# Kernel tuning notes

Hardware: AMD Instinct MI355X
Metric: run time of the kernel (lower is better)

## Reference

```python
import jax, jax.numpy as jnp
import numpy as np

H = 128
N_USER, N_PC, N_URL = 100000, 20000, 50000
E_UP, E_UU = 250000, 500000
NUM_LAYERS = 2


def _sage(x_src, x_dst, src_idx, dst_idx, n_dst, Wl, bl, Wr):
    # PyG SAGEConv (aggr='mean', root_weight=True, lin_r bias=False):
    # out = lin_l(mean_j x_src[j]) + lin_r(x_dst)
    msg = x_src[src_idx]                                   # [E, H] gather
    agg = jax.ops.segment_sum(msg, dst_idx, num_segments=n_dst)
    cnt = jax.ops.segment_sum(jnp.ones((src_idx.shape[0], 1), x_src.dtype),
                              dst_idx, num_segments=n_dst)
    mean = agg / jnp.maximum(cnt, 1.0)
    return mean @ Wl + bl + x_dst @ Wr


def setup_inputs() -> dict:
    key = jax.random.key(0)
    ks = jax.random.split(key, 24)
    s = 0.05
    inp = {
        'x_user': jax.random.normal(ks[0], (N_USER, 6), jnp.float32),
        'x_pc': jax.random.normal(ks[1], (N_PC, 4), jnp.float32),
        'x_url': jax.random.normal(ks[2], (N_URL, 3), jnp.float32),
        'edge_up_src': jax.random.randint(ks[3], (E_UP,), 0, N_USER, jnp.int32),
        'edge_up_dst': jax.random.randint(ks[4], (E_UP,), 0, N_PC, jnp.int32),
        'edge_uu_src': jax.random.randint(ks[5], (E_UU,), 0, N_USER, jnp.int32),
        'edge_uu_dst': jax.random.randint(ks[6], (E_UU,), 0, N_URL, jnp.int32),
        # input projections
        'Wu': jax.random.normal(ks[7], (6, H), jnp.float32) * s,
        'bu': jnp.zeros((H,), jnp.float32),
        'Wp': jax.random.normal(ks[8], (4, H), jnp.float32) * s,
        'bp': jnp.zeros((H,), jnp.float32),
        'Wr_feat': jax.random.normal(ks[9], (3, H), jnp.float32) * s,
        'br_feat': jnp.zeros((H,), jnp.float32),
        # SAGEConv params, stacked over layers [L, H, H]
        'Wl_pc': jax.random.normal(ks[10], (NUM_LAYERS, H, H), jnp.float32) * s,
        'bl_pc': jnp.zeros((NUM_LAYERS, H), jnp.float32),
        'Wr_pc': jax.random.normal(ks[11], (NUM_LAYERS, H, H), jnp.float32) * s,
        'Wl_url': jax.random.normal(ks[12], (NUM_LAYERS, H, H), jnp.float32) * s,
        'bl_url': jnp.zeros((NUM_LAYERS, H), jnp.float32),
        'Wr_url': jax.random.normal(ks[13], (NUM_LAYERS, H, H), jnp.float32) * s,
        # context aggregation + classifier
        'Wctx': jax.random.normal(ks[14], (3 * H, H), jnp.float32) * s,
        'bctx': jnp.zeros((H,), jnp.float32),
        'Wc1': jax.random.normal(ks[15], (H, H // 2), jnp.float32) * s,
        'bc1': jnp.zeros((H // 2,), jnp.float32),
        'Wc2': jax.random.normal(ks[16], (H // 2, 2), jnp.float32) * s,
        'bc2': jnp.zeros((2,), jnp.float32),
    }
    return inp


def reference(x_user, x_pc, x_url,
              edge_up_src, edge_up_dst, edge_uu_src, edge_uu_dst,
              Wu, bu, Wp, bp, Wr_feat, br_feat,
              Wl_pc, bl_pc, Wr_pc, Wl_url, bl_url, Wr_url,
              Wctx, bctx, Wc1, bc1, Wc2, bc2):
    user = x_user @ Wu + bu          # [N_USER, H] (never updated by convs)
    pc = x_pc @ Wp + bp              # [N_PC, H]
    url = x_url @ Wr_feat + br_feat  # [N_URL, H]

    for i in range(NUM_LAYERS):
        pc_new = _sage(user, pc, edge_up_src, edge_up_dst, pc.shape[0],
                       Wl_pc[i], bl_pc[i], Wr_pc[i])
        url_new = _sage(user, url, edge_uu_src, edge_uu_dst, url.shape[0],
                        Wl_url[i], bl_url[i], Wr_url[i])
        if i == 0:
            pc = jax.nn.relu(pc_new)
            url = jax.nn.relu(url_new)
        else:
            pc = jax.nn.relu(pc_new + pc)
            url = jax.nn.relu(url_new + url)

    # aggregate_resource_context: scatter-add of resource embeddings into users
    pc_ctx = jax.ops.segment_sum(pc[edge_up_dst], edge_up_src, num_segments=user.shape[0])
    url_ctx = jax.ops.segment_sum(url[edge_uu_dst], edge_uu_src, num_segments=user.shape[0])
    combined = jnp.concatenate([user, pc_ctx, url_ctx], axis=1)   # [N_USER, 3H]
    enriched = combined @ Wctx + bctx

    # classifier (dropout inactive at inference)
    h = jax.nn.relu(enriched @ Wc1 + bc1)
    return h @ Wc2 + bc2
```

## Files before the change

### kernel.cpp

```cpp
#include <hip/hip_runtime.h>

typedef unsigned short u16;
typedef short short8_t __attribute__((ext_vector_type(8)));
typedef float floatx4 __attribute__((ext_vector_type(4)));

static constexpr int N_USER_C = 100000;
static constexpr int N_PC_C   = 20000;
static constexpr int N_URL_C  = 50000;
static constexpr int E_UP_C   = 250000;
static constexpr int E_UU_C   = 500000;

static constexpr int S_UPD = 48;
static constexpr int S_UUD = 40;
static constexpr int S_SRC = 24;

__device__ __forceinline__ float bf2f(u16 h) {
    return __uint_as_float(((unsigned)h) << 16);
}
__device__ __forceinline__ u16 f2bf(float f) {
    unsigned u = __float_as_uint(f);
    u += 0x7fffu + ((u >> 16) & 1u);
    return (u16)(u >> 16);
}

struct PFArgs {
    const float* wsrc[12];
    u16* wdst;
    const float *Xu, *Wu, *bu, *Xp, *Wp, *bp, *Xr, *Wr, *br;
    u16 *ou, *op, *orr;
    const int *up_src, *up_dst, *uu_src, *uu_dst;
    int *cnt_up_dst, *cnt_uu_dst, *cnt_up_src, *cnt_uu_src;
    int *val_up_dst, *val_uu_dst;
    u16 *val_up_src, *val_uu_src;
};
__global__ __launch_bounds__(256) void prepfill_kernel(PFArgs a)
{
    int b = blockIdx.x, tid = threadIdx.x;
    if (b < 1960) {
        const int range = b & 7;
        const int ebase = (b >> 3) * 2048 + tid;
#pragma unroll
        for (int i = 0; i < 8; ++i) {
            int e = ebase + i * 256;
            if (e < E_UP_C) {
                int s = __builtin_nontemporal_load(a.up_src + e);
                int d = __builtin_nontemporal_load(a.up_dst + e);
                if (d / 2500 == range) {
                    int p = atomicAdd(&a.cnt_up_dst[d], 1);
                    if (p < S_UPD) a.val_up_dst[d * S_UPD + p] = s;
                }
                if (s / 12500 == range) {
                    int p = atomicAdd(&a.cnt_up_src[s], 1);
                    if (p < S_SRC) a.val_up_src[s * S_SRC + p] = (u16)d;
                }
            }
            if (e < E_UU_C) {
                int s = __builtin_nontemporal_load(a.uu_src + e);
                int d = __builtin_nontemporal_load(a.uu_dst + e);
                if (d / 6250 == range) {
                    int p = atomicAdd(&a.cnt_uu_dst[d], 1);
                    if (p < S_UUD) a.val_uu_dst[d * S_UUD + p] = s;
                }
                if (s / 12500 == range) {
                    int p = atomicAdd(&a.cnt_uu_src[s], 1);
                    if (p < S_SRC) a.val_uu_src[s * S_SRC + p] = (u16)d;
                }
            }
        }
    } else if (b < 1960 + 768) {
        int idx = (b - 1960) * 256 + tid;
        int m = idx >> 14, e = idx & 16383;
        int n = e >> 7, k = e & 127;
        int Nm = (m == 11) ? 64 : 128;
        u16 v = 0;
        if (n < Nm) v = f2bf(a.wsrc[m][k * Nm + n]);
        a.wdst[(size_t)m * 16384 + n * 128 + k] = v;
    } else {
        int idx = (b - 1960 - 768) * 256 + tid;
        const float* X; const float* W; const float* bi; u16* o; int K;
        if (idx < 1600000)       { X = a.Xu; W = a.Wu; bi = a.bu; o = a.ou; K = 6; }
        else if (idx < 1920000)  { idx -= 1600000; X = a.Xp; W = a.Wp; bi = a.bp; o = a.op; K = 4; }
        else                     { idx -= 1920000; X = a.Xr; W = a.Wr; bi = a.br; o = a.orr; K = 3; }
        int r = idx >> 4, c0 = (idx & 15) * 8;
        float acc[8];
        {
            const float4 b0 = *(const float4*)(bi + c0);
            const float4 b1 = *(const float4*)(bi + c0 + 4);
            acc[0] = b0.x; acc[1] = b0.y; acc[2] = b0.z; acc[3] = b0.w;
            acc[4] = b1.x; acc[5] = b1.y; acc[6] = b1.z; acc[7] = b1.w;
        }
        for (int k = 0; k < K; ++k) {
            float xk = X[(size_t)r * K + k];
            const float4 w0 = *(const float4*)(W + k * 128 + c0);
            const float4 w1 = *(const float4*)(W + k * 128 + c0 + 4);
            acc[0] += xk * w0.x; acc[1] += xk * w0.y; acc[2] += xk * w0.z; acc[3] += xk * w0.w;
            acc[4] += xk * w1.x; acc[5] += xk * w1.y; acc[6] += xk * w1.z; acc[7] += xk * w1.w;
        }
        uint4 pk;
        pk.x = (unsigned)f2bf(acc[0]) | ((unsigned)f2bf(acc[1]) << 16);
        pk.y = (unsigned)f2bf(acc[2]) | ((unsigned)f2bf(acc[3]) << 16);
        pk.z = (unsigned)f2bf(acc[4]) | ((unsigned)f2bf(acc[5]) << 16);
        pk.w = (unsigned)f2bf(acc[6]) | ((unsigned)f2bf(acc[7]) << 16);
        *(uint4*)(o + (size_t)r * 128 + c0) = pk;
    }
}

__device__ __forceinline__ void gm_row(
    const u16* __restrict__ feat, const int* __restrict__ cnt,
    const int* __restrict__ vals, int stride, u16* __restrict__ outp, int row, int lane)
{
    int deg = cnt[row];
    deg = __builtin_amdgcn_readfirstlane(deg);
    int n = deg < stride ? deg : stride;
    const int* vp = vals + row * stride;
    float a0 = 0.f, a1 = 0.f, b0 = 0.f, b1 = 0.f;
    float c0 = 0.f, c1 = 0.f, d0 = 0.f, d1 = 0.f;
    int j = 0;
    for (; j + 4 <= n; j += 4) {
        int i0 = __builtin_nontemporal_load(vp + j);
        int i1 = __builtin_nontemporal_load(vp + j + 1);
        int i2 = __builtin_nontemporal_load(vp + j + 2);
        int i3 = __builtin_nontemporal_load(vp + j + 3);
        unsigned u0 = *(const unsigned*)(feat + (size_t)i0 * 128 + lane * 2);
        unsigned u1 = *(const unsigned*)(feat + (size_t)i1 * 128 + lane * 2);
        unsigned u2 = *(const unsigned*)(feat + (size_t)i2 * 128 + lane * 2);
        unsigned u3 = *(const unsigned*)(feat + (size_t)i3 * 128 + lane * 2);
        a0 += bf2f((u16)(u0 & 0xffff)); a1 += bf2f((u16)(u0 >> 16));
        b0 += bf2f((u16)(u1 & 0xffff)); b1 += bf2f((u16)(u1 >> 16));
        c0 += bf2f((u16)(u2 & 0xffff)); c1 += bf2f((u16)(u2 >> 16));
        d0 += bf2f((u16)(u3 & 0xffff)); d1 += bf2f((u16)(u3 >> 16));
    }
    for (; j < n; ++j) {
        int i0 = __builtin_nontemporal_load(vp + j);
        unsigned u0 = *(const unsigned*)(feat + (size_t)i0 * 128 + lane * 2);
        a0 += bf2f((u16)(u0 & 0xffff)); a1 += bf2f((u16)(u0 >> 16));
    }
    float ax = (a0 + b0) + (c0 + d0), ay = (a1 + b1) + (c1 + d1);
    float inv = 1.0f / fmaxf((float)deg, 1.0f);
    unsigned o = (unsigned)f2bf(ax * inv) | ((unsigned)f2bf(ay * inv) << 16);
    *(unsigned*)(outp + (size_t)row * 128 + lane * 2) = o;
}

__global__ __launch_bounds__(256) void mean_ctx_kernel(
    const u16* __restrict__ feat,
    const int* __restrict__ cnt_pc, const int* __restrict__ val_pc, u16* __restrict__ out_pc,
    const int* __restrict__ cnt_url, const int* __restrict__ val_url, u16* __restrict__ out_url,
    const u16* __restrict__ Wctx_t, const float* __restrict__ bctx, u16* __restrict__ enr)
{
    __shared__ u16 Ws[2][128 * 40];
    const int b = blockIdx.x, tid = threadIdx.x;
    const int wave = tid >> 6, lane = tid & 63;

    if (b >= 782) {
        int bg = b - 782;
        if (bg < 5000) gm_row(feat, cnt_pc, val_pc, S_UPD, out_pc, bg * 4 + wave, lane);
        else           gm_row(feat, cnt_url, val_url, S_UUD, out_url, (bg - 5000) * 4 + wave, lane);
        return;
    }

    const int m = lane & 15, kq = lane >> 4;
    const int rbase = b * 128 + wave * 32;
    const int sn = tid >> 1, spart = tid & 1;
    const int M = N_USER_C;

    floatx4 acc[2][8];
#pragma unroll
    for (int mt = 0; mt < 2; ++mt)
#pragma unroll
        for (int nt = 0; nt < 8; ++nt) acc[mt][nt] = (floatx4)0.0f;

    auto stageW = [&](int kc, int buf) {
        *(short8_t*)&Ws[buf][sn * 40 + spart * 16] =
            *(const short8_t*)(Wctx_t + (size_t)sn * 128 + kc + spart * 16);
        *(short8_t*)&Ws[buf][sn * 40 + spart * 16 + 8] =
            *(const short8_t*)(Wctx_t + (size_t)sn * 128 + kc + spart * 16 + 8);
    };
    auto loadA = [&](int kc, int mt) -> short8_t {
        int row = rbase + mt * 16 + m; row = row < M ? row : M - 1;
        return *(const short8_t*)(feat + (size_t)row * 128 + kc + kq * 8);
    };

    stageW(0, 0);
    short8_t an0 = loadA(0, 0), an1 = loadA(0, 1);
    __syncthreads();
    for (int c = 0; c < 4; ++c) {
        int c1 = c + 1;
        if (c1 < 4) stageW(c1 * 32, c1 & 1);
        short8_t a0 = an0, a1 = an1;
        if (c1 < 4) { an0 = loadA(c1 * 32, 0); an1 = loadA(c1 * 32, 1); }
#pragma unroll
        for (int nt = 0; nt < 8; ++nt) {
            short8_t bb = *(const short8_t*)&Ws[c & 1][(nt * 16 + m) * 40 + kq * 8];
            acc[0][nt] = __builtin_amdgcn_mfma_f32_16x16x32_bf16(a0, bb, acc[0][nt], 0, 0, 0);
            acc[1][nt] = __builtin_amdgcn_mfma_f32_16x16x32_bf16(a1, bb, acc[1][nt], 0, 0, 0);
        }
        __syncthreads();
    }
#pragma unroll
    for (int nt = 0; nt < 8; ++nt) {
        int col = nt * 16 + m;
        float bv = bctx[col];
#pragma unroll
        for (int mt = 0; mt < 2; ++mt)
#pragma unroll
            for (int r = 0; r < 4; ++r) {
                int row = rbase + mt * 16 + kq * 4 + r;
                if (row < M) enr[(size_t)row * 128 + col] = f2bf(acc[mt][nt][r] + bv);
            }
    }
}

struct FSeg {
    const u16 *mean, *x0;
    const u16 *Wl0, *Wr0, *Wl1, *Wr1, *Wc;
    const float *b0, *b1;
    u16* out; int M; int bstart;
};
struct FArgs { FSeg s[2]; };

__global__ __launch_bounds__(256) void chain_kernel(FArgs fa)
{
    constexpr int XP = 136;
    __shared__ u16 Ws[2][128 * 40];
    __shared__ u16 Xs[128 * XP];

    int si = ((int)blockIdx.x >= fa.s[1].bstart) ? 1 : 0;
    FSeg sg = fa.s[si];
    const int bb = blockIdx.x - sg.bstart;

    const int tid = threadIdx.x;
    const int wave = tid >> 6, lane = tid & 63;
    const int m = lane & 15, kq = lane >> 4;
    const int rloc = wave * 32;
    const int rbase = bb * 128 + rloc;
    const int sn = tid >> 1, spart = tid & 1;

    floatx4 acc[2][8];

    auto zeroAcc = [&]() {
#pragma unroll
        for (int mt = 0; mt < 2; ++mt)
#pragma unroll
            for (int nt = 0; nt < 8; ++nt) acc[mt][nt] = (floatx4)0.0f;
    };
    auto stageW = [&](const u16* Wt, int kc, int buf) {
        *(short8_t*)&Ws[buf][sn * 40 + spart * 16] =
            *(const short8_t*)(Wt + (size_t)sn * 128 + kc + spart * 16);
        *(short8_t*)&Ws[buf][sn * 40 + spart * 16 + 8] =
            *(const short8_t*)(Wt + (size_t)sn * 128 + kc + spart * 16 + 8);
    };
    auto loadAg = [&](const u16* A, int kc, int mt) -> short8_t {
        int row = rbase + mt * 16 + m; row = row < sg.M ? row : sg.M - 1;
        return *(const short8_t*)(A + (size_t)row * 128 + kc + kq * 8);
    };
    auto loadAs = [&](int kc, int mt) -> short8_t {
        return *(const short8_t*)&Xs[(rloc + mt * 16 + m) * XP + kc + kq * 8];
    };
    auto mfmaChunk = [&](short8_t a0, short8_t a1, int buf) {
#pragma unroll
        for (int nt = 0; nt < 8; ++nt) {
            short8_t b = *(const short8_t*)&Ws[buf][(nt * 16 + m) * 40 + kq * 8];
            acc[0][nt] = __builtin_amdgcn_mfma_f32_16x16x32_bf16(a0, b, acc[0][nt], 0, 0, 0);
            acc[1][nt] = __builtin_amdgcn_mfma_f32_16x16x32_bf16(a1, b, acc[1][nt], 0, 0, 0);
        }
    };
    auto passDual = [&](const u16* W1, const u16* A1g, const u16* W2, const u16* A2g, bool a2lds) {
        zeroAcc();
        stageW(W1, 0, 0);
        short8_t an0 = loadAg(A1g, 0, 0), an1 = loadAg(A1g, 0, 1);
        __syncthreads();
        for (int c = 0; c < 8; ++c) {
            int c1 = c + 1;
            if (c1 < 8) {
                int kc1 = (c1 & 3) * 32;
                stageW(c1 < 4 ? W1 : W2, kc1, c1 & 1);
            }
            short8_t a0 = an0, a1 = an1;
            if (c1 < 8) {
                int kc1 = (c1 & 3) * 32;
                if (c1 < 4)     { an0 = loadAg(A1g, kc1, 0); an1 = loadAg(A1g, kc1, 1); }
                else if (a2lds) { an0 = loadAs(kc1, 0);      an1 = loadAs(kc1, 1); }
                else            { an0 = loadAg(A2g, kc1, 0); an1 = loadAg(A2g, kc1, 1); }
            }
            mfmaChunk(a0, a1, c & 1);
            __syncthreads();
        }
    };
    auto passSingleLds = [&](const u16* W1) {
        zeroAcc();
        stageW(W1, 0, 0);
        short8_t an0 = loadAs(0, 0), an1 = loadAs(0, 1);
        __syncthreads();
        for (int c = 0; c < 4; ++c) {
            int c1 = c + 1;
            if (c1 < 4) stageW(W1, c1 * 32, c1 & 1);
            short8_t a0 = an0, a1 = an1;
            if (c1 < 4) { an0 = loadAs(c1 * 32, 0); an1 = loadAs(c1 * 32, 1); }
            mfmaChunk(a0, a1, c & 1);
            __syncthreads();
        }
    };
    auto epilogueToLds = [&](const float* bias, bool addRes) {
#pragma unroll
        for (int nt = 0; nt < 8; ++nt) {
            int col = nt * 16 + m;
            float bv = bias[col];
#pragma unroll
            for (int mt = 0; mt < 2; ++mt)
#pragma unroll
                for (int r = 0; r < 4; ++r) {
                    int lrow = rloc + mt * 16 + kq * 4 + r;
                    float v = acc[mt][nt][r] + bv;
                    if (addRes) v += bf2f(Xs[lrow * XP + col]);
                    Xs[lrow * XP + col] = f2bf(fmaxf(v, 0.f));
                }
        }
        __syncthreads();
    };
    auto epilogueToGlobal = [&](u16* outp) {
#pragma unroll
        for (int nt = 0; nt < 8; ++nt) {
            int col = nt * 16 + m;
#pragma unroll
            for (int mt = 0; mt < 2; ++mt)
#pragma unroll
                for (int r = 0; r < 4; ++r) {
                    int row = rbase + mt * 16 + kq * 4 + r;
                    if (row < sg.M) outp[(size_t)row * 128 + col] = f2bf(acc[mt][nt][r]);
                }
        }
    };

    passDual(sg.Wl0, sg.mean, sg.Wr0, sg.x0, false);
    epilogueToLds(sg.b0, false);
    passDual(sg.Wl1, sg.mean, sg.Wr1, nullptr, true);
    epilogueToLds(sg.b1, true);
    passSingleLds(sg.Wc);
    epilogueToGlobal(sg.out);
}

__global__ __launch_bounds__(256) void ctx_final_kernel(
    const u16* __restrict__ enr,
    const int* __restrict__ cnt_up, const u16* __restrict__ val_up, const u16* __restrict__ pcW,
    const int* __restrict__ cnt_uu, const u16* __restrict__ val_uu, const u16* __restrict__ urlW,
    const u16* __restrict__ Wc1_t, const float* __restrict__ bc1,
    const float* __restrict__ Wc2, const float* __restrict__ bc2,
    float* __restrict__ out, int M)
{
    __shared__ u16 Xs[64 * 136];
    __shared__ u16 Wc1s[64 * 136];

    const int tid = threadIdx.x;
    const int wave = tid >> 6, lane = tid & 63;
    const int m = lane & 15, kq = lane >> 4;
    const int rbw = blockIdx.x * 64 + wave * 16;

    for (int idx = tid; idx < 64 * 16; idx += 256) {
        int row = idx >> 4, part = idx & 15;
        *(short8_t*)&Wc1s[row * 136 + part * 8] =
            *(const short8_t*)(Wc1_t + (size_t)row * 128 + part * 8);
    }

    for (int rr = 0; rr < 16; ++rr) {
        int row = rbw + rr;
        int lrow = wave * 16 + rr;
        unsigned o = 0;
        if (row < M) {
            int n0 = cnt_up[row], n1 = cnt_uu[row];
            n0 = __builtin_amdgcn_readfirstlane(n0); n1 = __builtin_amdgcn_readfirstlane(n1);
            n0 = n0 < S_SRC ? n0 : S_SRC; n1 = n1 < S_SRC ? n1 : S_SRC;
            int total = n0 + n1;
            const u16* vu = val_up + row * S_SRC;
            const u16* vr = val_uu + row * S_SRC;
            unsigned eu = *(const unsigned*)(enr + (size_t)row * 128 + lane * 2);
            float a0 = bf2f((u16)(eu & 0xffff)), a1 = bf2f((u16)(eu >> 16));
            float b0 = 0.f, b1 = 0.f, c0 = 0.f, c1 = 0.f, d0 = 0.f, d1 = 0.f;
            auto ld = [&](int t) -> unsigned {
                bool isup = t < n0;
                int idx = isup ? vu[t] : vr[t - n0];
                const u16* base = isup ? pcW : urlW;
                return *(const unsigned*)(base + (size_t)idx * 128 + lane * 2);
            };
            int t = 0;
            for (; t + 4 <= total; t += 4) {
                unsigned u0 = ld(t + 0), u1 = ld(t + 1), u2 = ld(t + 2), u3 = ld(t + 3);
                a0 += bf2f((u16)(u0 & 0xffff)); a1 += bf2f((u16)(u0 >> 16));
                b0 += bf2f((u16)(u1 & 0xffff)); b1 += bf2f((u16)(u1 >> 16));
                c0 += bf2f((u16)(u2 & 0xffff)); c1 += bf2f((u16)(u2 >> 16));
                d0 += bf2f((u16)(u3 & 0xffff)); d1 += bf2f((u16)(u3 >> 16));
            }
            for (; t < total; ++t) {
                unsigned u0 = ld(t);
                a0 += bf2f((u16)(u0 & 0xffff)); a1 += bf2f((u16)(u0 >> 16));
            }
            float ax = (a0 + b0) + (c0 + d0), ay = (a1 + b1) + (c1 + d1);
            o = (unsigned)f2bf(ax) | ((unsigned)f2bf(ay) << 16);
        }
        *(unsigned*)&Xs[lrow * 136 + 2 * lane] = o;
    }

    __syncthreads();

    floatx4 acc2[4];
#pragma unroll
    for (int nt = 0; nt < 4; ++nt) acc2[nt] = (floatx4)0.0f;
    for (int c = 0; c < 4; ++c) {
        int kc = c * 32;
        short8_t a = *(const short8_t*)&Xs[(wave * 16 + m) * 136 + kc + kq * 8];
#pragma unroll
        for (int nt = 0; nt < 4; ++nt) {
            short8_t b = *(const short8_t*)&Wc1s[(nt * 16 + m) * 136 + kc + kq * 8];
            acc2[nt] = __builtin_amdgcn_mfma_f32_16x16x32_bf16(a, b, acc2[nt], 0, 0, 0);
        }
    }

    float w0v[4], w1v[4], bv[4];
#pragma unroll
    for (int nt = 0; nt < 4; ++nt) {
        int col = nt * 16 + m;
        w0v[nt] = Wc2[col * 2 + 0];
        w1v[nt] = Wc2[col * 2 + 1];
        bv[nt]  = bc1[col];
    }
    float b20 = bc2[0], b21 = bc2[1];
#pragma unroll
    for (int r = 0; r < 4; ++r) {
        float o0 = 0.f, o1 = 0.f;
#pragma unroll
        for (int nt = 0; nt < 4; ++nt) {
            float v = acc2[nt][r] + bv[nt];
            v = fmaxf(v, 0.f);
            o0 += v * w0v[nt];
            o1 += v * w1v[nt];
        }
#pragma unroll
        for (int off = 1; off < 16; off <<= 1) {
            o0 += __shfl_xor(o0, off, 64);
            o1 += __shfl_xor(o1, off, 64);
        }
        if (m == 0) {
            int row = rbw + kq * 4 + r;
            if (row < M) {
                out[(size_t)row * 2 + 0] = o0 + b20;
                out[(size_t)row * 2 + 1] = o1 + b21;
            }
        }
    }
}

extern "C" void kernel_launch(void* const* d_in, const int* in_sizes, int n_in,
                              void* d_out, int out_size, void* d_ws, size_t ws_size,
                              hipStream_t stream)
{
    const float* x_user  = (const float*)d_in[0];
    const float* x_pc    = (const float*)d_in[1];
    const float* x_url   = (const float*)d_in[2];
    const int* e_up_src  = (const int*)d_in[3];
    const int* e_up_dst  = (const int*)d_in[4];
    const int* e_uu_src  = (const int*)d_in[5];
    const int* e_uu_dst  = (const int*)d_in[6];
    const float* Wu      = (const float*)d_in[7];
    const float* bu      = (const float*)d_in[8];
    const float* Wp      = (const float*)d_in[9];
    const float* bp      = (const float*)d_in[10];
    const float* Wr_feat = (const float*)d_in[11];
    const float* br_feat = (const float*)d_in[12];
    const float* Wl_pc   = (const float*)d_in[13];
    const float* bl_pc   = (const float*)d_in[14];
    const float* Wr_pc   = (const float*)d_in[15];
    const float* Wl_url  = (const float*)d_in[16];
    const float* bl_url  = (const float*)d_in[17];
    const float* Wr_url  = (const float*)d_in[18];
    const float* Wctx    = (const float*)d_in[19];
    const float* bctx    = (const float*)d_in[20];
    const float* Wc1     = (const float*)d_in[21];
    const float* bc1     = (const float*)d_in[22];
    const float* Wc2     = (const float*)d_in[23];
    const float* bc2     = (const float*)d_in[24];
    float* out = (float*)d_out;

    char* wsb = (char*)d_ws;
    u16* user_bf  = (u16*)(wsb);
    u16* enr      = (u16*)(wsb + 4ull *  6400000);
    u16* mean_pc  = (u16*)(wsb + 4ull * 12800000);
    u16* mean_url = (u16*)(wsb + 4ull * 14080000);
    u16* pc_a     = (u16*)(wsb + 4ull * 17280000);
    u16* pc_b     = (u16*)(wsb + 4ull * 18560000);
    u16* url_a    = (u16*)(wsb + 4ull * 19840000);
    u16* url_b    = (u16*)(wsb + 4ull * 23040000);
    u16* Wt       = (u16*)(wsb + 4ull * 26240000);
    int* cnts     = (int*)(wsb + 4ull * 26340000);
    int* up_dst_val = (int*)(wsb + 4ull * 26610000);
    int* uu_dst_val = (int*)(wsb + 4ull * 27570000);
    u16* up_src_val = (u16*)(wsb + 4ull * 29570000);
    u16* uu_src_val = (u16*)(wsb + 4ull * 30770000);

    int* cnt_up_dst = cnts + 0;
    int* cnt_uu_dst = cnts + 20000;
    int* cnt_up_src = cnts + 70000;
    int* cnt_uu_src = cnts + 170000;

    const int T = 256;

    hipMemsetAsync(cnts, 0, 270000ull * 4, stream);

    PFArgs pf;
    pf.wsrc[0] = Wl_pc;               pf.wsrc[1] = Wr_pc;
    pf.wsrc[2] = Wl_pc + 128 * 128;   pf.wsrc[3] = Wr_pc + 128 * 128;
    pf.wsrc[4] = Wl_url;              pf.wsrc[5] = Wr_url;
    pf.wsrc[6] = Wl_url + 128 * 128;  pf.wsrc[7] = Wr_url + 128 * 128;
    pf.wsrc[8] = Wctx;                pf.wsrc[9] = Wctx + 128 * 128;
    pf.wsrc[10] = Wctx + 256 * 128;   pf.wsrc[11] = Wc1;
    pf.wdst = Wt;
    pf.Xu = x_user; pf.Wu = Wu;      pf.bu = bu;      pf.ou = user_bf;
    pf.Xp = x_pc;   pf.Wp = Wp;      pf.bp = bp;      pf.op = pc_a;
    pf.Xr = x_url;  pf.Wr = Wr_feat; pf.br = br_feat; pf.orr = url_a;
    pf.up_src = e_up_src; pf.up_dst = e_up_dst;
    pf.uu_src = e_uu_src; pf.uu_dst = e_uu_dst;
    pf.cnt_up_dst = cnt_up_dst; pf.cnt_uu_dst = cnt_uu_dst;
    pf.cnt_up_src = cnt_up_src; pf.cnt_uu_src = cnt_uu_src;
    pf.val_up_dst = up_dst_val; pf.val_uu_dst = uu_dst_val;
    pf.val_up_src = up_src_val; pf.val_uu_src = uu_src_val;
    prepfill_kernel<<<1960 + 768 + 10625, T, 0, stream>>>(pf);

    mean_ctx_kernel<<<782 + 17500, T, 0, stream>>>(
        user_bf, cnt_up_dst, up_dst_val, mean_pc, cnt_uu_dst, uu_dst_val, mean_url,
        Wt + 8 * 16384, bctx, enr);

    FArgs fg;
    fg.s[0] = { mean_pc,  pc_a,  Wt + 0 * 16384, Wt + 1 * 16384, Wt + 2 * 16384, Wt + 3 * 16384,
                Wt + 9 * 16384,  bl_pc,  bl_pc + 128,  pc_b,  N_PC_C,   0 };
    fg.s[1] = { mean_url, url_a, Wt + 4 * 16384, Wt + 5 * 16384, Wt + 6 * 16384, Wt + 7 * 16384,
                Wt + 10 * 16384, bl_url, bl_url + 128, url_b, N_URL_C,  157 };
    chain_kernel<<<548, T, 0, stream>>>(fg);

    ctx_final_kernel<<<(N_USER_C + 63) / 64, T, 0, stream>>>(
        enr, cnt_up_src, up_src_val, pc_b, cnt_uu_src, uu_src_val, url_b,
        Wt + 11 * 16384, bc1, Wc2, bc2, out, N_USER_C);
}
```

Baseline: 433.1 us.

## Move user Wctx GEMM from gather kernel into fused chain GEMM kernel

The user-embedding x Wctx GEMM blocks are moved out of the gather-mean kernel, which now only does neighbor mean aggregation, and into the chain GEMM kernel as a third segment with a single-pass mode. This balances the workload between the memory-bound gather kernel and the compute-bound GEMM kernel and shrinks the gather kernel's shared-memory footprint, which may raise its occupancy. The risk is that the chain kernel grows from 548 to 1330 blocks. The GEMM now runs after the gathers instead of concurrently with them.

```diff
diff --git a/kernel.cpp b/kernel.cpp
--- a/kernel.cpp
+++ b/kernel.cpp
@@ -141,90 +141,34 @@
     *(unsigned*)(outp + (size_t)row * 128 + lane * 2) = o;
 }
 
-__global__ __launch_bounds__(256) void mean_ctx_kernel(
+__global__ __launch_bounds__(256) void gather_mean2_kernel(
     const u16* __restrict__ feat,
     const int* __restrict__ cnt_pc, const int* __restrict__ val_pc, u16* __restrict__ out_pc,
-    const int* __restrict__ cnt_url, const int* __restrict__ val_url, u16* __restrict__ out_url,
-    const u16* __restrict__ Wctx_t, const float* __restrict__ bctx, u16* __restrict__ enr)
-{
-    __shared__ u16 Ws[2][128 * 40];
-    const int b = blockIdx.x, tid = threadIdx.x;
-    const int wave = tid >> 6, lane = tid & 63;
-
-    if (b >= 782) {
-        int bg = b - 782;
-        if (bg < 5000) gm_row(feat, cnt_pc, val_pc, S_UPD, out_pc, bg * 4 + wave, lane);
-        else           gm_row(feat, cnt_url, val_url, S_UUD, out_url, (bg - 5000) * 4 + wave, lane);
-        return;
-    }
-
-    const int m = lane & 15, kq = lane >> 4;
-    const int rbase = b * 128 + wave * 32;
-    const int sn = tid >> 1, spart = tid & 1;
-    const int M = N_USER_C;
-
-    floatx4 acc[2][8];
-#pragma unroll
-    for (int mt = 0; mt < 2; ++mt)
-#pragma unroll
-        for (int nt = 0; nt < 8; ++nt) acc[mt][nt] = (floatx4)0.0f;
-
-    auto stageW = [&](int kc, int buf) {
-        *(short8_t*)&Ws[buf][sn * 40 + spart * 16] =
-            *(const short8_t*)(Wctx_t + (size_t)sn * 128 + kc + spart * 16);
-        *(short8_t*)&Ws[buf][sn * 40 + spart * 16 + 8] =
-            *(const short8_t*)(Wctx_t + (size_t)sn * 128 + kc + spart * 16 + 8);
-    };
-    auto loadA = [&](int kc, int mt) -> short8_t {
-        int row = rbase + mt * 16 + m; row = row < M ? row : M - 1;
-        return *(const short8_t*)(feat + (size_t)row * 128 + kc + kq * 8);
-    };
-
-    stageW(0, 0);
-    short8_t an0 = loadA(0, 0), an1 = loadA(0, 1);
-    __syncthreads();
-    for (int c = 0; c < 4; ++c) {
-        int c1 = c + 1;
-        if (c1 < 4) stageW(c1 * 32, c1 & 1);
-        short8_t a0 = an0, a1 = an1;
-        if (c1 < 4) { an0 = loadA(c1 * 32, 0); an1 = loadA(c1 * 32, 1); }
-#pragma unroll
-        for (int nt = 0; nt < 8; ++nt) {
-            short8_t bb = *(const short8_t*)&Ws[c & 1][(nt * 16 + m) * 40 + kq * 8];
-            acc[0][nt] = __builtin_amdgcn_mfma_f32_16x16x32_bf16(a0, bb, acc[0][nt], 0, 0, 0);
-            acc[1][nt] = __builtin_amdgcn_mfma_f32_16x16x32_bf16(a1, bb, acc[1][nt], 0, 0, 0);
-        }
-        __syncthreads();
-    }
-#pragma unroll
-    for (int nt = 0; nt < 8; ++nt) {
-        int col = nt * 16 + m;
-        float bv = bctx[col];
-#pragma unroll
-        for (int mt = 0; mt < 2; ++mt)
-#pragma unroll
-            for (int r = 0; r < 4; ++r) {
-                int row = rbase + mt * 16 + kq * 4 + r;
-                if (row < M) enr[(size_t)row * 128 + col] = f2bf(acc[mt][nt][r] + bv);
-            }
-    }
+    const int* __restrict__ cnt_url, const int* __restrict__ val_url, u16* __restrict__ out_url)
+{
+    int b = blockIdx.x;
+    int lane = threadIdx.x & 63, w = threadIdx.x >> 6;
+    if (b < 5000) gm_row(feat, cnt_pc, val_pc, S_UPD, out_pc, b * 4 + w, lane);
+    else          gm_row(feat, cnt_url, val_url, S_UUD, out_url, (b - 5000) * 4 + w, lane);
 }
 
 struct FSeg {
     const u16 *mean, *x0;
     const u16 *Wl0, *Wr0, *Wl1, *Wr1, *Wc;
     const float *b0, *b1;
-    u16* out; int M; int bstart;
+    u16* out; int M; int bstart; int mode;
 };
-struct FArgs { FSeg s[2]; };
-
-__global__ __launch_bounds__(256) void chain_kernel(FArgs fa)
+struct FArgs { FSeg s[3]; };
+
+__global__ __launch_bounds__(256) void gemm_fused_kernel(FArgs fa)
 {
     constexpr int XP = 136;
     __shared__ u16 Ws[2][128 * 40];
     __shared__ u16 Xs[128 * XP];
 
-    int si = ((int)blockIdx.x >= fa.s[1].bstart) ? 1 : 0;
+    int si = 0;
+    if ((int)blockIdx.x >= fa.s[1].bstart) si = 1;
+    if ((int)blockIdx.x >= fa.s[2].bstart) si = 2;
     FSeg sg = fa.s[si];
     const int bb = blockIdx.x - sg.bstart;
 
@@ -286,16 +230,21 @@
             __syncthreads();
         }
     };
-    auto passSingleLds = [&](const u16* W1) {
+    auto passSingle = [&](const u16* W1, const u16* A1g, bool lds) {
         zeroAcc();
         stageW(W1, 0, 0);
-        short8_t an0 = loadAs(0, 0), an1 = loadAs(0, 1);
+        short8_t an0, an1;
+        if (lds) { an0 = loadAs(0, 0); an1 = loadAs(0, 1); }
+        else     { an0 = loadAg(A1g, 0, 0); an1 = loadAg(A1g, 0, 1); }
         __syncthreads();
         for (int c = 0; c < 4; ++c) {
             int c1 = c + 1;
             if (c1 < 4) stageW(W1, c1 * 32, c1 & 1);
             short8_t a0 = an0, a1 = an1;
-            if (c1 < 4) { an0 = loadAs(c1 * 32, 0); an1 = loadAs(c1 * 32, 1); }
+            if (c1 < 4) {
+                if (lds) { an0 = loadAs(c1 * 32, 0); an1 = loadAs(c1 * 32, 1); }
+                else     { an0 = loadAg(A1g, c1 * 32, 0); an1 = loadAg(A1g, c1 * 32, 1); }
+            }
             mfmaChunk(a0, a1, c & 1);
             __syncthreads();
         }
@@ -317,26 +266,32 @@
         }
         __syncthreads();
     };
-    auto epilogueToGlobal = [&](u16* outp) {
+    auto epilogueToGlobal = [&](const float* bias, u16* outp) {
 #pragma unroll
         for (int nt = 0; nt < 8; ++nt) {
             int col = nt * 16 + m;
+            float bv = bias ? bias[col] : 0.0f;
 #pragma unroll
             for (int mt = 0; mt < 2; ++mt)
 #pragma unroll
                 for (int r = 0; r < 4; ++r) {
                     int row = rbase + mt * 16 + kq * 4 + r;
-                    if (row < sg.M) outp[(size_t)row * 128 + col] = f2bf(acc[mt][nt][r]);
-                }
-        }
-    };
-
-    passDual(sg.Wl0, sg.mean, sg.Wr0, sg.x0, false);
-    epilogueToLds(sg.b0, false);
-    passDual(sg.Wl1, sg.mean, sg.Wr1, nullptr, true);
-    epilogueToLds(sg.b1, true);
-    passSingleLds(sg.Wc);
-    epilogueToGlobal(sg.out);
+                    if (row < sg.M) outp[(size_t)row * 128 + col] = f2bf(acc[mt][nt][r] + bv);
+                }
+        }
+    };
+
+    if (sg.mode == 0) {
+        passDual(sg.Wl0, sg.mean, sg.Wr0, sg.x0, false);
+        epilogueToLds(sg.b0, false);
+        passDual(sg.Wl1, sg.mean, sg.Wr1, nullptr, true);
+        epilogueToLds(sg.b1, true);
+        passSingle(sg.Wc, nullptr, true);
+        epilogueToGlobal(nullptr, sg.out);
+    } else {
+        passSingle(sg.Wl0, sg.mean, false);
+        epilogueToGlobal(sg.b0, sg.out);
+    }
 }
 
 __global__ __launch_bounds__(256) void ctx_final_kernel(
@@ -523,16 +478,17 @@
     pf.val_up_src = up_src_val; pf.val_uu_src = uu_src_val;
     prepfill_kernel<<<1960 + 768 + 10625, T, 0, stream>>>(pf);
 
-    mean_ctx_kernel<<<782 + 17500, T, 0, stream>>>(
-        user_bf, cnt_up_dst, up_dst_val, mean_pc, cnt_uu_dst, uu_dst_val, mean_url,
-        Wt + 8 * 16384, bctx, enr);
+    gather_mean2_kernel<<<5000 + 12500, T, 0, stream>>>(
+        user_bf, cnt_up_dst, up_dst_val, mean_pc, cnt_uu_dst, uu_dst_val, mean_url);
 
     FArgs fg;
     fg.s[0] = { mean_pc,  pc_a,  Wt + 0 * 16384, Wt + 1 * 16384, Wt + 2 * 16384, Wt + 3 * 16384,
-                Wt + 9 * 16384,  bl_pc,  bl_pc + 128,  pc_b,  N_PC_C,   0 };
+                Wt + 9 * 16384,  bl_pc,  bl_pc + 128,  pc_b,  N_PC_C,   0,   0 };
     fg.s[1] = { mean_url, url_a, Wt + 4 * 16384, Wt + 5 * 16384, Wt + 6 * 16384, Wt + 7 * 16384,
-                Wt + 10 * 16384, bl_url, bl_url + 128, url_b, N_URL_C,  157 };
-    chain_kernel<<<548, T, 0, stream>>>(fg);
+                Wt + 10 * 16384, bl_url, bl_url + 128, url_b, N_URL_C,  157, 0 };
+    fg.s[2] = { user_bf,  nullptr, Wt + 8 * 16384, nullptr, nullptr, nullptr,
+                nullptr,         bctx,   nullptr,      enr,   N_USER_C, 548, 1 };
+    gemm_fused_kernel<<<548 + 782, T, 0, stream>>>(fg);
 
     ctx_final_kernel<<<(N_USER_C + 63) / 64, T, 0, stream>>>(
         enr, cnt_up_src, up_src_val, pc_b, cnt_uu_src, uu_src_val, url_b,
```

Result: faster. 373.8 us (-13.7%).
